# Kernel optimization log

Hardware: AMD Instinct MI355X
Metric: run time of the kernel (lower is better)

The kernel has to match this reference:

```python
import jax, jax.numpy as jnp
import numpy as np

D_MODEL = 1024
N_HEADS = 16


def setup_inputs() -> dict:
    key = jax.random.key(0)
    ks = jax.random.split(key, 11)
    B, L, D = 2, 2048, D_MODEL
    s = 1.0 / np.sqrt(D)
    return {
        "q": jax.random.normal(ks[0], (B, L, D), jnp.float32),
        "k": jax.random.normal(ks[1], (B, L, D), jnp.float32),
        "v": jax.random.normal(ks[2], (B, L, D), jnp.float32),
        "w_q": jax.random.normal(ks[3], (D, D), jnp.float32) * s,
        "b_q": jnp.zeros((D,), jnp.float32),
        "w_k": jax.random.normal(ks[4], (D, D), jnp.float32) * s,
        "b_k": jnp.zeros((D,), jnp.float32),
        "w_v": jax.random.normal(ks[5], (D, D), jnp.float32) * s,
        "b_v": jnp.zeros((D,), jnp.float32),
        "w_o": jax.random.normal(ks[6], (D, D), jnp.float32) * s,
        "b_o": jnp.zeros((D,), jnp.float32),
    }


def reference(q, k, v, w_q, b_q, w_k, b_k, w_v, b_v, w_o, b_o):
    B, L, D = q.shape
    H = N_HEADS
    d_h = D // H
    # QKV projections (nn.Linear: x @ W^T + b)
    qh = (q @ w_q.T + b_q).reshape(B, L, H, d_h).transpose(0, 2, 1, 3)  # [B,H,L,d_h]
    kh = (k @ w_k.T + b_k).reshape(B, L, H, d_h).transpose(0, 2, 1, 3)
    vh = (v @ w_v.T + b_v).reshape(B, L, H, d_h).transpose(0, 2, 1, 3)
    # scaled dot-product attention
    scores = jnp.einsum('bhqd,bhkd->bhqk', qh, kh) / jnp.sqrt(jnp.float32(d_h))
    attn = jax.nn.softmax(scores, axis=-1)                               # [B,H,L,L]
    ctx = jnp.einsum('bhqk,bhkd->bhqd', attn, vh)                        # [B,H,L,d_h]
    ctx = ctx.transpose(0, 2, 1, 3).reshape(B, L, D)
    out = ctx @ w_o.T + b_o
    return out, attn
```

## Files before the change

kernel.cpp:

```cpp
#include <hip/hip_runtime.h>
#include <hip/hip_bf16.h>
#include <stdint.h>

#define DEV static __device__ __forceinline__

typedef float f32x4 __attribute__((ext_vector_type(4)));
typedef __bf16 bf16x8 __attribute__((ext_vector_type(8)));
typedef unsigned short u16x8 __attribute__((ext_vector_type(8)));
typedef unsigned short u16x4 __attribute__((ext_vector_type(4)));
typedef uint32_t u32x4 __attribute__((ext_vector_type(4)));
typedef unsigned short u16;

#define B_ 2
#define L_ 2048
#define D_MODEL_ 1024
#define H_ 16
#define DH_ 64

#define SHIFT2 11.5415603f

DEV u16 f2bf(float f) {
  union { float f; uint32_t u; } v; v.f = f;
  uint32_t r = v.u + 0x7FFFu + ((v.u >> 16) & 1u);
  return (u16)(r >> 16);
}

DEV float exp2v(float x) {
#if __has_builtin(__builtin_amdgcn_exp2f)
  return __builtin_amdgcn_exp2f(x);
#else
  float r;
  asm("v_exp_f32 %0, %1" : "=v"(r) : "v"(x));
  return r;
#endif
}

DEV uint32_t pkbf(float a, float b) {
  __hip_bfloat162 h = __float22bfloat162_rn(float2{a, b});
  union { __hip_bfloat162 h; uint32_t u; } cv; cv.h = h;
  return cv.u;
}

DEV f32x4 mfma16(bf16x8 a, bf16x8 b, f32x4 c) {
  return __builtin_amdgcn_mfma_f32_16x16x32_bf16(a, b, c, 0, 0, 0);
}

DEV void gl_lds16(const void* g, void* l) {
  __builtin_amdgcn_global_load_lds(
      (const __attribute__((address_space(1))) unsigned int*)g,
      (__attribute__((address_space(3))) unsigned int*)l, 16, 0, 0);
}

struct CastArgs {
  const float* src[7];
  u16* dst[7];
  int n8[7];
};

__global__ __launch_bounds__(256) void cast_kernel(CastArgs a) {
  const int z = blockIdx.z;
  u16* d = a.dst[z];
  const int n8 = a.n8[z];
  const int stride = gridDim.x * blockDim.x;
  const float* s = a.src[z];
  for (int i = blockIdx.x * blockDim.x + threadIdx.x; i < n8; i += stride) {
    const float4* sp = (const float4*)s + (size_t)i * 2;
    float4 x0 = sp[0], x1 = sp[1];
    u16x8 o;
    o[0] = f2bf(x0.x); o[1] = f2bf(x0.y); o[2] = f2bf(x0.z); o[3] = f2bf(x0.w);
    o[4] = f2bf(x1.x); o[5] = f2bf(x1.y); o[6] = f2bf(x1.z); o[7] = f2bf(x1.w);
    *((u16x8*)d + i) = o;
  }
}

#define GM 4096
#define GN 1024
#define GK 1024

struct GemmArgs {
  const u16* X[3];
  const u16* W[3];
  const float* bias[3];
  void* out[3];
  float alpha[3];
  int mode[3];
};

__global__ __launch_bounds__(256) void gemm_bt(GemmArgs g) {
  const int z = blockIdx.z;
  const u16* X = g.X[z];
  const u16* W = g.W[z];
  const float* bias = g.bias[z];
  const float alpha = g.alpha[z];
  const int mode = g.mode[z];
  const int m0 = blockIdx.y * 128, n0 = blockIdx.x * 128;

  __shared__ __align__(16) char smem[32 * 1024];
  char* As = smem;
  char* Bs = smem + 16 * 1024;

  const int tid = threadIdx.x;
  const int lane = tid & 63, w = tid >> 6;
  const int l15 = lane & 15, l4 = lane >> 4;
  const int wm = (w >> 1) * 64, wn = (w & 1) * 64;

  f32x4 acc[4][4];
#pragma unroll
  for (int i = 0; i < 4; ++i)
#pragma unroll
    for (int j = 0; j < 4; ++j) acc[i][j] = f32x4{0.f, 0.f, 0.f, 0.f};

  for (int ks = 0; ks < GK; ks += 64) {
    __syncthreads();
    for (int c = w; c < 16; c += 4) {
      int r = c * 8 + (lane >> 3);
      int j = lane & 7;
      int sj = j ^ (r & 7);
      gl_lds16((const char*)(X + (size_t)(m0 + r) * GK + ks) + sj * 16, As + c * 1024);
      gl_lds16((const char*)(W + (size_t)(n0 + r) * GK + ks) + sj * 16, Bs + c * 1024);
    }
    __syncthreads();
#pragma unroll
    for (int ksub = 0; ksub < 2; ++ksub) {
      bf16x8 af[4], bfr[4];
#pragma unroll
      for (int mf = 0; mf < 4; ++mf) {
        int r = wm + mf * 16 + l15;
        int j16 = ksub * 4 + l4;
        af[mf] = *(const bf16x8*)(As + r * 128 + ((j16 ^ (r & 7)) * 16));
      }
#pragma unroll
      for (int nf = 0; nf < 4; ++nf) {
        int r = wn + nf * 16 + l15;
        int j16 = ksub * 4 + l4;
        bfr[nf] = *(const bf16x8*)(Bs + r * 128 + ((j16 ^ (r & 7)) * 16));
      }
#pragma unroll
      for (int mf = 0; mf < 4; ++mf)
#pragma unroll
        for (int nf = 0; nf < 4; ++nf) acc[mf][nf] = mfma16(af[mf], bfr[nf], acc[mf][nf]);
    }
  }

  if (mode == 2) {
    u16* base = (u16*)g.out[z];
#pragma unroll
    for (int nf = 0; nf < 4; ++nf) {
      int n = n0 + wn + nf * 16 + l15;
      float bv = bias[n];
      int df = (n & 63) >> 4, fl15 = n & 15, hh = n >> 6;
#pragma unroll
      for (int mf = 0; mf < 4; ++mf) {
        int m = m0 + wm + mf * 16 + l4 * 4;
        u16x4 pk;
#pragma unroll
        for (int r = 0; r < 4; ++r) pk[r] = f2bf((acc[mf][nf][r] + bv) * alpha);
        int lg = m & 2047, bb = m >> 11;
        int t = lg >> 6, lc = lg & 63;
        int c = lc >> 3, e = lc & 7;
        size_t off = ((((size_t)(bb * H_ + hh) * 32 + t) * 8 + (c >> 2) * 4 + df) * 512) +
                     ((c & 3) * 16 + fl15) * 8 + e;
        *(u16x4*)(base + off) = pk;
      }
    }
  } else if (mode == 3) {
    u16* base = (u16*)g.out[z];
#pragma unroll
    for (int nf = 0; nf < 4; ++nf) {
      int n = n0 + wn + nf * 16 + l15;
      float bv = bias[n];
      int dh = n & 63, hh = n >> 6;
      int c = dh >> 3;
      int fragb = (c >> 2) * 4, laneb = (c & 3) * 16, e = dh & 7;
#pragma unroll
      for (int mf = 0; mf < 4; ++mf) {
#pragma unroll
        for (int r = 0; r < 4; ++r) {
          int m = m0 + wm + mf * 16 + l4 * 4 + r;
          int lg = m & 2047, bb = m >> 11;
          int t = lg >> 6, nfk = (lg >> 4) & 3, l15k = lg & 15;
          size_t off = ((((size_t)(bb * H_ + hh) * 32 + t) * 8 + fragb + nfk) * 512) +
                       (laneb + l15k) * 8 + e;
          base[off] = f2bf((acc[mf][nf][r] + bv) * alpha);
        }
      }
    }
  } else {
#pragma unroll
    for (int nf = 0; nf < 4; ++nf) {
      int n = n0 + wn + nf * 16 + l15;
      float bv = bias[n];
#pragma unroll
      for (int mf = 0; mf < 4; ++mf) {
#pragma unroll
        for (int r = 0; r < 4; ++r) {
          int m = m0 + wm + mf * 16 + l4 * 4 + r;
          float val = (acc[mf][nf][r] + bv) * alpha;
          if (mode == 1)
            ((float*)g.out[z])[(size_t)m * GN + n] = val;
          else
            ((u16*)g.out[z])[(size_t)m * GN + n] = f2bf(val);
        }
      }
    }
  }
}

__global__ __launch_bounds__(256) void attn_kernel(const u16* Qp, const u16* KF,
                                                   const u16* VF, float* attn,
                                                   u16* ctx) {
  const int bid = blockIdx.x;
  const int lid = (bid & 7) * 128 + (bid >> 3);
  const int q0 = (lid & 31) * 64;
  const int h = (lid >> 5) & 15;
  const int b = lid >> 9;
  const int tid = threadIdx.x, lane = tid & 63, w = tid >> 6;
  const int l15 = lane & 15, l4 = lane >> 4;

  __shared__ __align__(16) char smem[16 * 1024];
  char* Pw = smem + w * 4096;

  const u16* Qbase = Qp + ((size_t)(b * L_ + q0 + w * 16) * D_MODEL_ + h * DH_);
  const u16* Kf = KF + ((size_t)(b * H_ + h) * 32) * 4096;
  const u16* Vb = VF + ((size_t)(b * H_ + h) * 32) * 4096;
  float* attnb = attn + ((size_t)(b * H_ + h)) * L_ * L_;

  bf16x8 qa[2];
#pragma unroll
  for (int ksub = 0; ksub < 2; ++ksub)
    qa[ksub] = *(const bf16x8*)(Qbase + (size_t)l15 * D_MODEL_ + (ksub * 4 + l4) * 8);

  f32x4 sa0 = {0.f, 0.f, 0.f, 0.f}, sa1 = {0.f, 0.f, 0.f, 0.f};
  for (int t = 0; t < 32; ++t) {
    const u16* Kt = Kf + (size_t)t * 4096;
    bf16x8 kb[2][4];
#pragma unroll
    for (int ksub = 0; ksub < 2; ++ksub)
#pragma unroll
      for (int i = 0; i < 4; ++i)
        kb[ksub][i] = *(const bf16x8*)(Kt + (ksub * 4 + i) * 512 + lane * 8);
    f32x4 s[4];
#pragma unroll
    for (int nf = 0; nf < 4; ++nf) s[nf] = f32x4{0.f, 0.f, 0.f, 0.f};
    __builtin_amdgcn_s_setprio(1);
#pragma unroll
    for (int ksub = 0; ksub < 2; ++ksub)
#pragma unroll
      for (int nf = 0; nf < 4; ++nf) s[nf] = mfma16(kb[ksub][nf], qa[ksub], s[nf]);
    __builtin_amdgcn_s_setprio(0);
#pragma unroll
    for (int r = 0; r < 4; ++r) {
      float e0 = exp2v(s[0][r] - SHIFT2), e1 = exp2v(s[1][r] - SHIFT2);
      float e2 = exp2v(s[2][r] - SHIFT2), e3 = exp2v(s[3][r] - SHIFT2);
      sa0[r] += (e0 + e1);
      sa1[r] += (e2 + e3);
    }
  }
  float ssum = (sa0[0] + sa0[1]) + (sa0[2] + sa0[3]) +
               (sa1[0] + sa1[1]) + (sa1[2] + sa1[3]);
  ssum += __shfl_xor(ssum, 16);
  ssum += __shfl_xor(ssum, 32);
  const float c2 = SHIFT2 + __log2f(ssum);

  f32x4 cacc[4];
#pragma unroll
  for (int i = 0; i < 4; ++i) cacc[i] = f32x4{0.f, 0.f, 0.f, 0.f};

  const int swz = l15 & 7;
  float* awave = attnb + (size_t)(q0 + w * 16) * L_;

  for (int t = 0; t < 32; ++t) {
    const int c0 = t * 64;
    const u16* Kt = Kf + (size_t)t * 4096;
    const u16* Vt = Vb + (size_t)t * 4096;
    bf16x8 kb[2][4], va[2][4];
#pragma unroll
    for (int ksub = 0; ksub < 2; ++ksub)
#pragma unroll
      for (int i = 0; i < 4; ++i) {
        kb[ksub][i] = *(const bf16x8*)(Kt + (ksub * 4 + i) * 512 + lane * 8);
        va[ksub][i] = *(const bf16x8*)(Vt + (ksub * 4 + i) * 512 + lane * 8);
      }

    f32x4 s[4];
#pragma unroll
    for (int nf = 0; nf < 4; ++nf) s[nf] = f32x4{0.f, 0.f, 0.f, 0.f};
    __builtin_amdgcn_s_setprio(1);
#pragma unroll
    for (int ksub = 0; ksub < 2; ++ksub)
#pragma unroll
      for (int nf = 0; nf < 4; ++nf) s[nf] = mfma16(kb[ksub][nf], qa[ksub], s[nf]);
    __builtin_amdgcn_s_setprio(0);

#pragma unroll
    for (int nf = 0; nf < 4; ++nf) {
      f32x4 p4;
#pragma unroll
      for (int r = 0; r < 4; ++r) p4[r] = exp2v(s[nf][r] - c2);
      *(f32x4*)(Pw + l15 * 256 + (((nf * 4 + l4) ^ swz) * 16)) = p4;
    }
#pragma unroll
    for (int j = 0; j < 4; ++j) {
      int row = 4 * j + (lane >> 4);
      f32x4 v = *(const f32x4*)(Pw + row * 256 + (((lane & 15) ^ (row & 7)) * 16));
      __builtin_nontemporal_store(
          v, (f32x4*)(awave + (size_t)row * L_ + c0 + (lane & 15) * 4));
    }
    __builtin_amdgcn_s_setprio(1);
#pragma unroll
    for (int ksub = 0; ksub < 2; ++ksub) {
      int cbase = (ksub * 4 + l4) * 2;
      f32x4 plo = *(const f32x4*)(Pw + l15 * 256 + ((cbase ^ swz) * 16));
      f32x4 phi = *(const f32x4*)(Pw + l15 * 256 + (((cbase + 1) ^ swz) * 16));
      union { u32x4 u; bf16x8 h; } pa;
      pa.u[0] = pkbf(plo[0], plo[1]);
      pa.u[1] = pkbf(plo[2], plo[3]);
      pa.u[2] = pkbf(phi[0], phi[1]);
      pa.u[3] = pkbf(phi[2], phi[3]);
#pragma unroll
      for (int df = 0; df < 4; ++df)
        cacc[df] = mfma16(pa.h, va[ksub][df], cacc[df]);
    }
    __builtin_amdgcn_s_setprio(0);
  }

#pragma unroll
  for (int df = 0; df < 4; ++df) {
#pragma unroll
    for (int r = 0; r < 4; ++r) {
      int row = q0 + w * 16 + l4 * 4 + r;
      int col = h * DH_ + df * 16 + l15;
      ctx[(size_t)(b * L_ + row) * D_MODEL_ + col] = f2bf(cacc[df][r]);
    }
  }
}

extern "C" void kernel_launch(void* const* d_in, const int* in_sizes, int n_in,
                              void* d_out, int out_size, void* d_ws, size_t ws_size,
                              hipStream_t stream) {
  const float* q = (const float*)d_in[0];
  const float* k = (const float*)d_in[1];
  const float* v = (const float*)d_in[2];
  const float* w_q = (const float*)d_in[3];
  const float* b_q = (const float*)d_in[4];
  const float* w_k = (const float*)d_in[5];
  const float* b_k = (const float*)d_in[6];
  const float* w_v = (const float*)d_in[7];
  const float* b_v = (const float*)d_in[8];
  const float* w_o = (const float*)d_in[9];
  const float* b_o = (const float*)d_in[10];

  float* out = (float*)d_out;
  float* attn = (float*)d_out + (size_t)B_ * L_ * D_MODEL_;

  const size_t MB = 1u << 20;
  char* ws = (char*)d_ws;
  u16* qb = (u16*)(ws + 0 * MB);
  u16* kb = (u16*)(ws + 8 * MB);
  u16* vb = (u16*)(ws + 16 * MB);
  u16* wqb = (u16*)(ws + 24 * MB);
  u16* wkb = (u16*)(ws + 26 * MB);
  u16* wvb = (u16*)(ws + 28 * MB);
  u16* wob = (u16*)(ws + 30 * MB);
  u16* Qp = (u16*)(ws + 32 * MB);
  u16* KF = (u16*)(ws + 40 * MB);
  u16* VF = (u16*)(ws + 48 * MB);
  u16* ctx = kb;

  CastArgs ca;
  ca.src[0] = q;   ca.dst[0] = qb;  ca.n8[0] = (B_ * L_ * D_MODEL_) / 8;
  ca.src[1] = k;   ca.dst[1] = kb;  ca.n8[1] = (B_ * L_ * D_MODEL_) / 8;
  ca.src[2] = v;   ca.dst[2] = vb;  ca.n8[2] = (B_ * L_ * D_MODEL_) / 8;
  ca.src[3] = w_q; ca.dst[3] = wqb; ca.n8[3] = (D_MODEL_ * D_MODEL_) / 8;
  ca.src[4] = w_k; ca.dst[4] = wkb; ca.n8[4] = (D_MODEL_ * D_MODEL_) / 8;
  ca.src[5] = w_v; ca.dst[5] = wvb; ca.n8[5] = (D_MODEL_ * D_MODEL_) / 8;
  ca.src[6] = w_o; ca.dst[6] = wob; ca.n8[6] = (D_MODEL_ * D_MODEL_) / 8;
  cast_kernel<<<dim3(1024, 1, 7), 256, 0, stream>>>(ca);

  GemmArgs ga;
  ga.X[0] = qb;  ga.W[0] = wqb; ga.bias[0] = b_q; ga.out[0] = Qp; ga.alpha[0] = 0.125f * 1.44269504f; ga.mode[0] = 0;
  ga.X[1] = kb;  ga.W[1] = wkb; ga.bias[1] = b_k; ga.out[1] = KF; ga.alpha[1] = 1.f;    ga.mode[1] = 3;
  ga.X[2] = vb;  ga.W[2] = wvb; ga.bias[2] = b_v; ga.out[2] = VF; ga.alpha[2] = 1.f;    ga.mode[2] = 2;
  gemm_bt<<<dim3(8, 32, 3), 256, 0, stream>>>(ga);

  attn_kernel<<<dim3(1024, 1, 1), 256, 0, stream>>>(Qp, KF, VF, attn, ctx);

  GemmArgs go;
  go.X[0] = ctx; go.W[0] = wob; go.bias[0] = b_o; go.out[0] = out; go.alpha[0] = 1.f; go.mode[0] = 1;
  go.X[1] = ctx; go.W[1] = wob; go.bias[1] = b_o; go.out[1] = out; go.alpha[1] = 1.f; go.mode[1] = 1;
  go.X[2] = ctx; go.W[2] = wob; go.bias[2] = b_o; go.out[2] = out; go.alpha[2] = 1.f; go.mode[2] = 1;
  gemm_bt<<<dim3(8, 32, 1), 256, 0, stream>>>(go);
}
```

Baseline: 230.7 us.

## Process two 16-row query groups per wave to reuse K/V fragment loads

Result: no change. 230.6 us (-0.0%).

```diff
diff --git a/kernel.cpp b/kernel.cpp
--- a/kernel.cpp
+++ b/kernel.cpp
@@ -210,27 +210,35 @@
                                                    const u16* VF, float* attn,
                                                    u16* ctx) {
   const int bid = blockIdx.x;
-  const int lid = (bid & 7) * 128 + (bid >> 3);
-  const int q0 = (lid & 31) * 64;
-  const int h = (lid >> 5) & 15;
-  const int b = lid >> 9;
+  const int lid = (bid & 7) * 64 + (bid >> 3);
+  const int q0 = (lid & 15) * 128;
+  const int h = (lid >> 4) & 15;
+  const int b = lid >> 8;
   const int tid = threadIdx.x, lane = tid & 63, w = tid >> 6;
   const int l15 = lane & 15, l4 = lane >> 4;
 
   __shared__ __align__(16) char smem[16 * 1024];
   char* Pw = smem + w * 4096;
 
-  const u16* Qbase = Qp + ((size_t)(b * L_ + q0 + w * 16) * D_MODEL_ + h * DH_);
+  const u16* Qbase = Qp + ((size_t)(b * L_ + q0 + w * 32) * D_MODEL_ + h * DH_);
   const u16* Kf = KF + ((size_t)(b * H_ + h) * 32) * 4096;
   const u16* Vb = VF + ((size_t)(b * H_ + h) * 32) * 4096;
   float* attnb = attn + ((size_t)(b * H_ + h)) * L_ * L_;
 
-  bf16x8 qa[2];
-#pragma unroll
-  for (int ksub = 0; ksub < 2; ++ksub)
-    qa[ksub] = *(const bf16x8*)(Qbase + (size_t)l15 * D_MODEL_ + (ksub * 4 + l4) * 8);
-
-  f32x4 sa0 = {0.f, 0.f, 0.f, 0.f}, sa1 = {0.f, 0.f, 0.f, 0.f};
+  bf16x8 qa[2][2];
+#pragma unroll
+  for (int gq = 0; gq < 2; ++gq)
+#pragma unroll
+    for (int ksub = 0; ksub < 2; ++ksub)
+      qa[gq][ksub] = *(const bf16x8*)(Qbase + (size_t)(gq * 16 + l15) * D_MODEL_ +
+                                      (ksub * 4 + l4) * 8);
+
+  f32x4 sa[2][2];
+#pragma unroll
+  for (int gq = 0; gq < 2; ++gq) {
+    sa[gq][0] = f32x4{0.f, 0.f, 0.f, 0.f};
+    sa[gq][1] = f32x4{0.f, 0.f, 0.f, 0.f};
+  }
   for (int t = 0; t < 32; ++t) {
     const u16* Kt = Kf + (size_t)t * 4096;
     bf16x8 kb[2][4];
@@ -239,35 +247,43 @@
 #pragma unroll
       for (int i = 0; i < 4; ++i)
         kb[ksub][i] = *(const bf16x8*)(Kt + (ksub * 4 + i) * 512 + lane * 8);
-    f32x4 s[4];
-#pragma unroll
-    for (int nf = 0; nf < 4; ++nf) s[nf] = f32x4{0.f, 0.f, 0.f, 0.f};
-    __builtin_amdgcn_s_setprio(1);
-#pragma unroll
-    for (int ksub = 0; ksub < 2; ++ksub)
-#pragma unroll
-      for (int nf = 0; nf < 4; ++nf) s[nf] = mfma16(kb[ksub][nf], qa[ksub], s[nf]);
-    __builtin_amdgcn_s_setprio(0);
-#pragma unroll
-    for (int r = 0; r < 4; ++r) {
-      float e0 = exp2v(s[0][r] - SHIFT2), e1 = exp2v(s[1][r] - SHIFT2);
-      float e2 = exp2v(s[2][r] - SHIFT2), e3 = exp2v(s[3][r] - SHIFT2);
-      sa0[r] += (e0 + e1);
-      sa1[r] += (e2 + e3);
-    }
-  }
-  float ssum = (sa0[0] + sa0[1]) + (sa0[2] + sa0[3]) +
-               (sa1[0] + sa1[1]) + (sa1[2] + sa1[3]);
-  ssum += __shfl_xor(ssum, 16);
-  ssum += __shfl_xor(ssum, 32);
-  const float c2 = SHIFT2 + __log2f(ssum);
-
-  f32x4 cacc[4];
-#pragma unroll
-  for (int i = 0; i < 4; ++i) cacc[i] = f32x4{0.f, 0.f, 0.f, 0.f};
+#pragma unroll
+    for (int gq = 0; gq < 2; ++gq) {
+      f32x4 s[4];
+#pragma unroll
+      for (int nf = 0; nf < 4; ++nf) s[nf] = f32x4{0.f, 0.f, 0.f, 0.f};
+      __builtin_amdgcn_s_setprio(1);
+#pragma unroll
+      for (int ksub = 0; ksub < 2; ++ksub)
+#pragma unroll
+        for (int nf = 0; nf < 4; ++nf) s[nf] = mfma16(kb[ksub][nf], qa[gq][ksub], s[nf]);
+      __builtin_amdgcn_s_setprio(0);
+#pragma unroll
+      for (int r = 0; r < 4; ++r) {
+        float e0 = exp2v(s[0][r] - SHIFT2), e1 = exp2v(s[1][r] - SHIFT2);
+        float e2 = exp2v(s[2][r] - SHIFT2), e3 = exp2v(s[3][r] - SHIFT2);
+        sa[gq][0][r] += (e0 + e1);
+        sa[gq][1][r] += (e2 + e3);
+      }
+    }
+  }
+  float c2[2];
+#pragma unroll
+  for (int gq = 0; gq < 2; ++gq) {
+    float ssum = (sa[gq][0][0] + sa[gq][0][1]) + (sa[gq][0][2] + sa[gq][0][3]) +
+                 (sa[gq][1][0] + sa[gq][1][1]) + (sa[gq][1][2] + sa[gq][1][3]);
+    ssum += __shfl_xor(ssum, 16);
+    ssum += __shfl_xor(ssum, 32);
+    c2[gq] = SHIFT2 + __log2f(ssum);
+  }
+
+  f32x4 cacc[2][4];
+#pragma unroll
+  for (int gq = 0; gq < 2; ++gq)
+#pragma unroll
+    for (int i = 0; i < 4; ++i) cacc[gq][i] = f32x4{0.f, 0.f, 0.f, 0.f};
 
   const int swz = l15 & 7;
-  float* awave = attnb + (size_t)(q0 + w * 16) * L_;
 
   for (int t = 0; t < 32; ++t) {
     const int c0 = t * 64;
@@ -282,57 +298,63 @@
         va[ksub][i] = *(const bf16x8*)(Vt + (ksub * 4 + i) * 512 + lane * 8);
       }
 
-    f32x4 s[4];
-#pragma unroll
-    for (int nf = 0; nf < 4; ++nf) s[nf] = f32x4{0.f, 0.f, 0.f, 0.f};
-    __builtin_amdgcn_s_setprio(1);
-#pragma unroll
-    for (int ksub = 0; ksub < 2; ++ksub)
-#pragma unroll
-      for (int nf = 0; nf < 4; ++nf) s[nf] = mfma16(kb[ksub][nf], qa[ksub], s[nf]);
-    __builtin_amdgcn_s_setprio(0);
-
-#pragma unroll
-    for (int nf = 0; nf < 4; ++nf) {
-      f32x4 p4;
-#pragma unroll
-      for (int r = 0; r < 4; ++r) p4[r] = exp2v(s[nf][r] - c2);
-      *(f32x4*)(Pw + l15 * 256 + (((nf * 4 + l4) ^ swz) * 16)) = p4;
-    }
-#pragma unroll
-    for (int j = 0; j < 4; ++j) {
-      int row = 4 * j + (lane >> 4);
-      f32x4 v = *(const f32x4*)(Pw + row * 256 + (((lane & 15) ^ (row & 7)) * 16));
-      __builtin_nontemporal_store(
-          v, (f32x4*)(awave + (size_t)row * L_ + c0 + (lane & 15) * 4));
-    }
-    __builtin_amdgcn_s_setprio(1);
-#pragma unroll
-    for (int ksub = 0; ksub < 2; ++ksub) {
-      int cbase = (ksub * 4 + l4) * 2;
-      f32x4 plo = *(const f32x4*)(Pw + l15 * 256 + ((cbase ^ swz) * 16));
-      f32x4 phi = *(const f32x4*)(Pw + l15 * 256 + (((cbase + 1) ^ swz) * 16));
-      union { u32x4 u; bf16x8 h; } pa;
-      pa.u[0] = pkbf(plo[0], plo[1]);
-      pa.u[1] = pkbf(plo[2], plo[3]);
-      pa.u[2] = pkbf(phi[0], phi[1]);
-      pa.u[3] = pkbf(phi[2], phi[3]);
-#pragma unroll
-      for (int df = 0; df < 4; ++df)
-        cacc[df] = mfma16(pa.h, va[ksub][df], cacc[df]);
-    }
-    __builtin_amdgcn_s_setprio(0);
-  }
-
-#pragma unroll
-  for (int df = 0; df < 4; ++df) {
-#pragma unroll
-    for (int r = 0; r < 4; ++r) {
-      int row = q0 + w * 16 + l4 * 4 + r;
-      int col = h * DH_ + df * 16 + l15;
-      ctx[(size_t)(b * L_ + row) * D_MODEL_ + col] = f2bf(cacc[df][r]);
-    }
-  }
+#pragma unroll
+    for (int gq = 0; gq < 2; ++gq) {
+      f32x4 s[4];
+#pragma unroll
+      for (int nf = 0; nf < 4; ++nf) s[nf] = f32x4{0.f, 0.f, 0.f, 0.f};
+      __builtin_amdgcn_s_setprio(1);
+#pragma unroll
+      for (int ksub = 0; ksub < 2; ++ksub)
+#pragma unroll
+        for (int nf = 0; nf < 4; ++nf) s[nf] = mfma16(kb[ksub][nf], qa[gq][ksub], s[nf]);
+      __builtin_amdgcn_s_setprio(0);
+
+#pragma unroll
+      for (int nf = 0; nf < 4; ++nf) {
+        f32x4 p4;
+#pragma unroll
+        for (int r = 0; r < 4; ++r) p4[r] = exp2v(s[nf][r] - c2[gq]);
+        *(f32x4*)(Pw + l15 * 256 + (((nf * 4 + l4) ^ swz) * 16)) = p4;
+      }
+      float* awave = attnb + (size_t)(q0 + w * 32 + gq * 16) * L_;
+#pragma unroll
+      for (int j = 0; j < 4; ++j) {
+        int row = 4 * j + (lane >> 4);
+        f32x4 v = *(const f32x4*)(Pw + row * 256 + (((lane & 15) ^ (row & 7)) * 16));
+        __builtin_nontemporal_store(
+            v, (f32x4*)(awave + (size_t)row * L_ + c0 + (lane & 15) * 4));
+      }
+      __builtin_amdgcn_s_setprio(1);
+#pragma unroll
+      for (int ksub = 0; ksub < 2; ++ksub) {
+        int cbase = (ksub * 4 + l4) * 2;
+        f32x4 plo = *(const f32x4*)(Pw + l15 * 256 + ((cbase ^ swz) * 16));
+        f32x4 phi = *(const f32x4*)(Pw + l15 * 256 + (((cbase + 1) ^ swz) * 16));
+        union { u32x4 u; bf16x8 h; } pa;
+        pa.u[0] = pkbf(plo[0], plo[1]);
+        pa.u[1] = pkbf(plo[2], plo[3]);
+        pa.u[2] = pkbf(phi[0], phi[1]);
+        pa.u[3] = pkbf(phi[2], phi[3]);
+#pragma unroll
+        for (int df = 0; df < 4; ++df)
+          cacc[gq][df] = mfma16(pa.h, va[ksub][df], cacc[gq][df]);
+      }
+      __builtin_amdgcn_s_setprio(0);
+    }
+  }
+
+#pragma unroll
+  for (int gq = 0; gq < 2; ++gq)
+#pragma unroll
+    for (int df = 0; df < 4; ++df) {
+#pragma unroll
+      for (int r = 0; r < 4; ++r) {
+        int row = q0 + w * 32 + gq * 16 + l4 * 4 + r;
+        int col = h * DH_ + df * 16 + l15;
+        ctx[(size_t)(b * L_ + row) * D_MODEL_ + col] = f2bf(cacc[gq][df][r]);
+      }
+    }
 }
 
 extern "C" void kernel_launch(void* const* d_in, const int* in_sizes, int n_in,
@@ -383,7 +405,7 @@
   ga.X[2] = vb;  ga.W[2] = wvb; ga.bias[2] = b_v; ga.out[2] = VF; ga.alpha[2] = 1.f;    ga.mode[2] = 2;
   gemm_bt<<<dim3(8, 32, 3), 256, 0, stream>>>(ga);
 
-  attn_kernel<<<dim3(1024, 1, 1), 256, 0, stream>>>(Qp, KF, VF, attn, ctx);
+  attn_kernel<<<dim3(512, 1, 1), 256, 0, stream>>>(Qp, KF, VF, attn, ctx);
 
   GemmArgs go;
   go.X[0] = ctx; go.W[0] = wob; go.bias[0] = b_o; go.out[0] = out; go.alpha[0] = 1.f; go.mode[0] = 1;
```
